# Optimization experiments

Hardware: AMD Instinct MI355X
Metric: run time of the kernel (lower is better)

Reference implementation:

```python
import jax, jax.numpy as jnp
import numpy as np

N = 262144          # total nodes in batched graph
B = 2048            # number of graphs
IN_DIM = 512        # in_dim == hidden_dim (required by GRUCell usage)
HID = 512
OUT_DIM = 128
TIMESTEPS = 2


def setup_inputs() -> dict:
    key = jax.random.key(0)
    ks = jax.random.split(key, 12)
    s = 0.02
    x = jax.random.normal(ks[0], (N, IN_DIM), dtype=jnp.float32)
    # sorted random segment ids: ragged graph sizes, node -> graph id
    segment_ids = jnp.sort(jax.random.randint(ks[1], (N,), 0, B, dtype=jnp.int32))
    return {
        "x": x,
        "segment_ids": segment_ids,
        "w_att_l": jax.random.normal(ks[2], (IN_DIM,), dtype=jnp.float32) * s,
        "w_att_r": jax.random.normal(ks[3], (IN_DIM,), dtype=jnp.float32) * s,
        "W_node": jax.random.normal(ks[4], (IN_DIM, HID), dtype=jnp.float32) * s,
        "W_ih": jax.random.normal(ks[5], (3 * HID, HID), dtype=jnp.float32) * s,
        "W_hh": jax.random.normal(ks[6], (3 * HID, HID), dtype=jnp.float32) * s,
        "b_ih": jax.random.normal(ks[7], (3 * HID,), dtype=jnp.float32) * s,
        "b_hh": jax.random.normal(ks[8], (3 * HID,), dtype=jnp.float32) * s,
        "W_lin": jax.random.normal(ks[9], (HID, OUT_DIM), dtype=jnp.float32) * s,
        "b_lin": jax.random.normal(ks[10], (OUT_DIM,), dtype=jnp.float32) * s,
    }


def _segment_softmax(alpha, seg, num_segments):
    # numerically stable per-graph softmax over nodes
    m = jax.ops.segment_max(alpha, seg, num_segments=num_segments)
    e = jnp.exp(alpha - m[seg])
    denom = jax.ops.segment_sum(e, seg, num_segments=num_segments)
    return e / denom[seg]


def _gru_cell(inp, h, W_ih, W_hh, b_ih, b_hh):
    gi = inp @ W_ih.T + b_ih          # [B, 3H]
    gh = h @ W_hh.T + b_hh            # [B, 3H]
    gi_r, gi_z, gi_n = jnp.split(gi, 3, axis=-1)
    gh_r, gh_z, gh_n = jnp.split(gh, 3, axis=-1)
    r = jax.nn.sigmoid(gi_r + gh_r)
    z = jax.nn.sigmoid(gi_z + gh_z)
    n = jnp.tanh(gi_n + r * gh_n)
    return (1.0 - z) * n + z * h


def reference(x, segment_ids, w_att_l, w_att_r, W_node, W_ih, W_hh, b_ih, b_hh, W_lin, b_lin):
    seg = segment_ids
    # SumPooling: per-graph sum of node features -> initial GRU hidden state
    out = jax.ops.segment_sum(x, seg, num_segments=B)      # [B, IN_DIM]
    # src_feats (x) are constant across timesteps -> precompute projections
    left_att = x @ w_att_l                                  # [N]
    h_neighbors = x @ W_node                                # [N, HID]
    for _ in range(TIMESTEPS):
        right_att = out @ w_att_r                           # [B]
        alpha = jax.nn.leaky_relu(left_att + right_att[seg], negative_slope=0.01)
        scores = _segment_softmax(alpha, seg, B)            # [N]
        msg = h_neighbors * scores[:, None]                 # [N, HID]
        gat_out = jax.ops.segment_sum(msg, seg, num_segments=B)  # [B, HID]
        h = jax.nn.elu(gat_out)
        # dropout is identity in eval mode
        out = jax.nn.silu(_gru_cell(h, out, W_ih, W_hh, b_ih, b_hh))
    return out @ W_lin + b_lin                              # [B, OUT_DIM]
```

## Files before the change

kernel.cpp:

```cpp
#include <hip/hip_runtime.h>
#include <hip/hip_bf16.h>
#include <cstdint>
#include <cstddef>

#define N_NODES 262144
#define NGRAPH  2048
#define DIM     512
#define HID3    1536
#define OUTD    128

typedef __attribute__((ext_vector_type(8))) short  short8;
typedef __attribute__((ext_vector_type(4))) float  floatx4;
typedef __attribute__((ext_vector_type(2))) float  floatx2;

__device__ inline unsigned short f2bf(float f) {
    union { float f; uint32_t u; } v; v.f = f;
    uint32_t u = v.u;
    return (unsigned short)((u + 0x7fffu + ((u >> 16) & 1u)) >> 16);
}
__device__ inline float bf2f(unsigned short h) {
    union { uint32_t u; float f; } v; v.u = ((uint32_t)h) << 16; return v.f;
}

__device__ __forceinline__ void gload_lds16(const void* g, void* l) {
    __builtin_amdgcn_global_load_lds((const __attribute__((address_space(1))) void*)g,
                                     (__attribute__((address_space(3))) void*)l, 16, 0, 0);
}

__device__ __forceinline__ int lbound(const int* __restrict__ seg, int b) {
    int lo = 0, hi = N_NODES;
    while (lo < hi) { int mid = (lo + hi) >> 1; if (seg[mid] < b) lo = mid + 1; else hi = mid; }
    return lo;
}

template<bool WRITE_XQ>
__global__ __launch_bounds__(256) void k_init(const float* __restrict__ x,
        const int* __restrict__ seg, const float* __restrict__ watl,
        const float* __restrict__ Wih, const float* __restrict__ Whh,
        const float* __restrict__ Wnode,
        float* __restrict__ left_att, float* __restrict__ hcur,
        unsigned short* __restrict__ hcur_bf, unsigned char* __restrict__ xq,
        unsigned short* __restrict__ Wihb, unsigned short* __restrict__ Whhb,
        unsigned short* __restrict__ WnT, int* __restrict__ starts) {
    int t = threadIdx.x;
    int bid = blockIdx.x;

    if (bid >= 3584) {
        __shared__ float tile[32][33];
        int idx = bid - 3584;
        int bx = idx >> 4, by = idx & 15;
        int tx = t & 31, ty = t >> 5;
        #pragma unroll
        for (int r = 0; r < 32; r += 8)
            tile[ty + r][tx] = Wnode[(size_t)(bx * 32 + ty + r) * DIM + by * 32 + tx];
        __syncthreads();
        #pragma unroll
        for (int r = 0; r < 32; r += 8)
            WnT[(size_t)(by * 32 + ty + r) * DIM + bx * 32 + tx] = f2bf(tile[tx][ty + r]);
        return;
    }
    if (bid >= 2048) {
        int isW2 = bid >= 2816;
        int i4 = (bid - (isW2 ? 2816 : 2048)) * 256 + t;
        const float* src = isW2 ? Whh : Wih;
        unsigned short* dst = isW2 ? Whhb : Wihb;
        floatx4 a = *reinterpret_cast<const floatx4*>(src + (size_t)i4 * 4);
        ushort4 o;
        o.x = f2bf(a[0]); o.y = f2bf(a[1]); o.z = f2bf(a[2]); o.w = f2bf(a[3]);
        *reinterpret_cast<ushort4*>(dst + (size_t)i4 * 4) = o;
        return;
    }

    __shared__ float wl[DIM];
    __shared__ float red[4 * DIM];
    int b = bid;
    wl[t] = watl[t]; wl[t + 256] = watl[t + 256];
    int s = lbound(seg, b), e = lbound(seg, b + 1);
    if (t == 0) {
        starts[b] = s;
        if (b == NGRAPH - 1) starts[NGRAPH] = e;
    }
    __syncthreads();
    int w = t >> 6, lane = t & 63;
    int f0 = lane * 4;
    float acc[8] = {0.f,0.f,0.f,0.f,0.f,0.f,0.f,0.f};

    auto proc = [&](int i, floatx4 v0, floatx4 v1) {
        acc[0] += v0[0]; acc[1] += v0[1]; acc[2] += v0[2]; acc[3] += v0[3];
        acc[4] += v1[0]; acc[5] += v1[1]; acc[6] += v1[2]; acc[7] += v1[3];
        float dot = v0[0]*wl[f0] + v0[1]*wl[f0+1] + v0[2]*wl[f0+2] + v0[3]*wl[f0+3]
                  + v1[0]*wl[256+f0] + v1[1]*wl[256+f0+1] + v1[2]*wl[256+f0+2] + v1[3]*wl[256+f0+3];
        #pragma unroll
        for (int off = 32; off > 0; off >>= 1) dot += __shfl_xor(dot, off);
        if (lane == 0) left_att[i] = dot;
        if constexpr (WRITE_XQ) {
            unsigned int q0 = (unsigned int)__builtin_amdgcn_cvt_pk_fp8_f32(v0[0], v0[1], 0, false);
            q0 = (unsigned int)__builtin_amdgcn_cvt_pk_fp8_f32(v0[2], v0[3], (int)q0, true);
            unsigned int q1 = (unsigned int)__builtin_amdgcn_cvt_pk_fp8_f32(v1[0], v1[1], 0, false);
            q1 = (unsigned int)__builtin_amdgcn_cvt_pk_fp8_f32(v1[2], v1[3], (int)q1, true);
            *reinterpret_cast<unsigned int*>(xq + (size_t)i * DIM + f0) = q0;
            *reinterpret_cast<unsigned int*>(xq + (size_t)i * DIM + 256 + f0) = q1;
        }
    };

    int i = s + w;
    for (; i + 4 < e; i += 8) {
        floatx4 a0 = __builtin_nontemporal_load(reinterpret_cast<const floatx4*>(x + (size_t)i * DIM + f0));
        floatx4 a1 = __builtin_nontemporal_load(reinterpret_cast<const floatx4*>(x + (size_t)i * DIM + 256 + f0));
        floatx4 b0 = __builtin_nontemporal_load(reinterpret_cast<const floatx4*>(x + (size_t)(i + 4) * DIM + f0));
        floatx4 b1 = __builtin_nontemporal_load(reinterpret_cast<const floatx4*>(x + (size_t)(i + 4) * DIM + 256 + f0));
        proc(i, a0, a1);
        proc(i + 4, b0, b1);
    }
    if (i < e) {
        floatx4 a0 = __builtin_nontemporal_load(reinterpret_cast<const floatx4*>(x + (size_t)i * DIM + f0));
        floatx4 a1 = __builtin_nontemporal_load(reinterpret_cast<const floatx4*>(x + (size_t)i * DIM + 256 + f0));
        proc(i, a0, a1);
    }

    #pragma unroll
    for (int j = 0; j < 4; j++) {
        red[w * DIM + f0 + j]       = acc[j];
        red[w * DIM + 256 + f0 + j] = acc[4 + j];
    }
    __syncthreads();
    float s0 = red[t]       + red[DIM + t]       + red[2*DIM + t]       + red[3*DIM + t];
    float s1 = red[256 + t] + red[DIM + 256 + t] + red[2*DIM + 256 + t] + red[3*DIM + 256 + t];
    hcur[(size_t)b * DIM + t] = s0;
    hcur[(size_t)b * DIM + 256 + t] = s1;
    hcur_bf[(size_t)b * DIM + t] = f2bf(s0);
    hcur_bf[(size_t)b * DIM + 256 + t] = f2bf(s1);
}

template<bool XQ, bool FUSE_GATE>
__global__ __launch_bounds__(256) void k_att(const float* __restrict__ x,
        const unsigned char* __restrict__ xq, const float* __restrict__ left,
        const int* __restrict__ starts, float* __restrict__ hcur,
        unsigned short* __restrict__ hcurbf,
        const float* __restrict__ gi, const float* __restrict__ gh,
        const float* __restrict__ bih, const float* __restrict__ bhh,
        const float* __restrict__ watr, unsigned short* __restrict__ swbf) {
    __shared__ float red[4 * DIM];
    __shared__ float rsh[4];
    __shared__ float rsm[4];
    __shared__ float rscal[4];
    int b = blockIdx.x, t = threadIdx.x;
    int w = t >> 6, lane = t & 63;

    float p;
    if constexpr (FUSE_GATE) {
        size_t gb = (size_t)b * HID3;
        float o01[2];
        #pragma unroll
        for (int half = 0; half < 2; ++half) {
            int j = t + half * 256;
            float gir = gi[gb + j]        + bih[j];
            float giz = gi[gb + 512 + j]  + bih[512 + j];
            float gin = gi[gb + 1024 + j] + bih[1024 + j];
            float ghr = gh[gb + j]        + bhh[j];
            float ghz = gh[gb + 512 + j]  + bhh[512 + j];
            float ghn = gh[gb + 1024 + j] + bhh[1024 + j];
            float rg = 1.0f / (1.0f + __expf(-(gir + ghr)));
            float zg = 1.0f / (1.0f + __expf(-(giz + ghz)));
            float nn = tanhf(gin + rg * ghn);
            float hp = hcur[(size_t)b * DIM + j];
            float nh = (1.0f - zg) * nn + zg * hp;
            float o = nh / (1.0f + __expf(-nh));
            hcur[(size_t)b * DIM + j] = o;
            hcurbf[(size_t)b * DIM + j] = f2bf(o);
            o01[half] = o;
        }
        p = o01[0] * watr[t] + o01[1] * watr[t + 256];
    } else {
        p = hcur[(size_t)b * DIM + t] * watr[t] + hcur[(size_t)b * DIM + 256 + t] * watr[256 + t];
    }
    #pragma unroll
    for (int off = 32; off > 0; off >>= 1) p += __shfl_xor(p, off);
    if (lane == 0) rsh[w] = p;
    int s = starts[b], e = starts[b + 1];
    __syncthreads();
    float ra = rsh[0] + rsh[1] + rsh[2] + rsh[3];

    float m = -1e30f;
    for (int i = s + t; i < e; i += 256) {
        float a = left[i] + ra; a = a >= 0.f ? a : 0.01f * a;
        m = fmaxf(m, a);
    }
    #pragma unroll
    for (int off = 32; off > 0; off >>= 1) m = fmaxf(m, __shfl_xor(m, off));
    if (lane == 0) rsm[w] = m;
    __syncthreads();
    m = fmaxf(fmaxf(rsm[0], rsm[1]), fmaxf(rsm[2], rsm[3]));

    float acc[8] = {0.f,0.f,0.f,0.f,0.f,0.f,0.f,0.f};
    float esum = 0.f;
    if constexpr (XQ) {
        int f0 = lane * 8;
        auto qacc = [&](uint2 q, float ev) {
            floatx2 p0 = __builtin_amdgcn_cvt_pk_f32_fp8((int)q.x, false);
            floatx2 p1 = __builtin_amdgcn_cvt_pk_f32_fp8((int)q.x, true);
            floatx2 p2 = __builtin_amdgcn_cvt_pk_f32_fp8((int)q.y, false);
            floatx2 p3 = __builtin_amdgcn_cvt_pk_f32_fp8((int)q.y, true);
            acc[0] += ev * p0[0]; acc[1] += ev * p0[1];
            acc[2] += ev * p1[0]; acc[3] += ev * p1[1];
            acc[4] += ev * p2[0]; acc[5] += ev * p2[1];
            acc[6] += ev * p3[0]; acc[7] += ev * p3[1];
        };
        int i = s + w;
        for (; i + 4 < e; i += 8) {
            uint2 q0 = *reinterpret_cast<const uint2*>(xq + (size_t)i * DIM + f0);
            uint2 q1 = *reinterpret_cast<const uint2*>(xq + (size_t)(i + 4) * DIM + f0);
            float a0 = left[i] + ra;     a0 = a0 >= 0.f ? a0 : 0.01f * a0;
            float a1 = left[i + 4] + ra; a1 = a1 >= 0.f ? a1 : 0.01f * a1;
            float e0 = __expf(a0 - m), e1 = __expf(a1 - m);
            esum += e0 + e1;
            qacc(q0, e0);
            qacc(q1, e1);
        }
        if (i < e) {
            uint2 q0 = *reinterpret_cast<const uint2*>(xq + (size_t)i * DIM + f0);
            float a0 = left[i] + ra; a0 = a0 >= 0.f ? a0 : 0.01f * a0;
            float e0 = __expf(a0 - m);
            esum += e0;
            qacc(q0, e0);
        }
        #pragma unroll
        for (int j = 0; j < 8; j++) red[w * DIM + f0 + j] = acc[j];
    } else {
        int f0 = lane * 4;
        for (int i = s + w; i < e; i += 4) {
            float a0 = left[i] + ra; a0 = a0 >= 0.f ? a0 : 0.01f * a0;
            float e0 = __expf(a0 - m);
            esum += e0;
            float4 v0 = *reinterpret_cast<const float4*>(x + (size_t)i * DIM + f0);
            float4 v1 = *reinterpret_cast<const float4*>(x + (size_t)i * DIM + 256 + f0);
            acc[0] += e0 * v0.x; acc[1] += e0 * v0.y; acc[2] += e0 * v0.z; acc[3] += e0 * v0.w;
            acc[4] += e0 * v1.x; acc[5] += e0 * v1.y; acc[6] += e0 * v1.z; acc[7] += e0 * v1.w;
        }
        #pragma unroll
        for (int j = 0; j < 4; j++) {
            red[w * DIM + f0 + j]       = acc[j];
            red[w * DIM + 256 + f0 + j] = acc[4 + j];
        }
    }
    #pragma unroll
    for (int off = 32; off > 0; off >>= 1) esum += __shfl_xor(esum, off);
    if (lane == 0) rscal[w] = esum;
    __syncthreads();
    float tot = rscal[0] + rscal[1] + rscal[2] + rscal[3];
    float inv = tot > 0.f ? 1.0f / tot : 0.0f;
    float s0 = (red[t]       + red[DIM + t]       + red[2*DIM + t]       + red[3*DIM + t])       * inv;
    float s1 = (red[256 + t] + red[DIM + 256 + t] + red[2*DIM + 256 + t] + red[3*DIM + 256 + t]) * inv;
    swbf[(size_t)b * DIM + t] = f2bf(s0);
    swbf[(size_t)b * DIM + 256 + t] = f2bf(s1);
}

__global__ __launch_bounds__(256, 2) void k_gemm(const unsigned short* __restrict__ A0,
        const unsigned short* __restrict__ Wt0, float* __restrict__ Cf0,
        unsigned short* __restrict__ Cb0, int Ncols0, int ny0,
        const unsigned short* __restrict__ A1, const unsigned short* __restrict__ Wt1,
        float* __restrict__ Cf1, unsigned short* __restrict__ Cb1, int Ncols1) {
    const int z = blockIdx.z;
    if (z == 0 && (int)blockIdx.y >= ny0) return;
    const unsigned short* A  = z ? A1  : A0;
    const unsigned short* Wt = z ? Wt1 : Wt0;
    float* Cf          = z ? Cf1 : Cf0;
    unsigned short* Cb = z ? Cb1 : Cb0;
    const int Ncols    = z ? Ncols1 : Ncols0;

    __shared__ __align__(16) unsigned short lA[2][128 * 64];
    __shared__ __align__(16) unsigned short lW[2][128 * 64];

    int t = threadIdx.x;
    int w = t >> 6, lane = t & 63;
    int wr = w >> 1, wc = w & 1;
    int mbase = blockIdx.x * 128;
    int nbase = blockIdx.y * 128;
    int fr = lane & 15, hi = lane >> 4;
    int swz_r = (fr & 7) << 4;

    int rbase = t >> 3;
    int cole = ((((t & 7) * 16) ^ ((rbase & 7) << 4)) >> 1);
    int ldsoff = t * 16;

    floatx4 acc[4][4];
    #pragma unroll
    for (int m = 0; m < 4; m++)
        #pragma unroll
        for (int n = 0; n < 4; n++) {
            acc[m][n][0] = 0.f; acc[m][n][1] = 0.f; acc[m][n][2] = 0.f; acc[m][n][3] = 0.f;
        }

    const unsigned short* gA = A  + (size_t)(mbase + rbase) * DIM + cole;
    const unsigned short* gW = Wt + (size_t)(nbase + rbase) * DIM + cole;

    auto stage = [&](int kk, int buf) {
        #pragma unroll
        for (int c = 0; c < 4; ++c) {
            gload_lds16(gA + (size_t)(c * 32) * DIM + kk, (char*)&lA[buf][0] + c * 4096 + ldsoff);
            gload_lds16(gW + (size_t)(c * 32) * DIM + kk, (char*)&lW[buf][0] + c * 4096 + ldsoff);
        }
    };

    stage(0, 0);
    __syncthreads();
    int cur = 0;
    for (int it = 0; it < 8; ++it) {
        if (it < 7) stage((it + 1) * 64, cur ^ 1);
        #pragma unroll
        for (int ks = 0; ks < 2; ++ks) {
            short8 af[4], bf[4];
            int bc = (ks * 64 + hi * 16) ^ swz_r;
            #pragma unroll
            for (int m = 0; m < 4; ++m) {
                int row = wr * 64 + m * 16 + fr;
                af[m] = *reinterpret_cast<const short8*>(&lA[cur][(row * 128 + bc) >> 1]);
            }
            #pragma unroll
            for (int n = 0; n < 4; ++n) {
                int row = wc * 64 + n * 16 + fr;
                bf[n] = *reinterpret_cast<const short8*>(&lW[cur][(row * 128 + bc) >> 1]);
            }
            #pragma unroll
            for (int m = 0; m < 4; ++m)
                #pragma unroll
                for (int n = 0; n < 4; ++n)
                    acc[m][n] = __builtin_amdgcn_mfma_f32_16x16x32_bf16(af[m], bf[n], acc[m][n], 0, 0, 0);
        }
        if (it < 7) __syncthreads();
        cur ^= 1;
    }

    int rq = hi * 4;
    #pragma unroll
    for (int m = 0; m < 4; m++) {
        #pragma unroll
        for (int n = 0; n < 4; n++) {
            int col = nbase + wc * 64 + n * 16 + fr;
            #pragma unroll
            for (int r = 0; r < 4; r++) {
                int row = mbase + wr * 64 + m * 16 + rq + r;
                float v = acc[m][n][r];
                if (Cb) {
                    v = v > 0.f ? v : (__expf(v) - 1.0f);
                    Cb[(size_t)row * Ncols + col] = f2bf(v);
                } else {
                    Cf[(size_t)row * Ncols + col] = v;
                }
            }
        }
    }
}

__global__ __launch_bounds__(128) void k_fin(const float* __restrict__ hcur,
        const float* __restrict__ gi, const float* __restrict__ gh,
        const float* __restrict__ bih, const float* __restrict__ bhh,
        const float* __restrict__ Wlin, const float* __restrict__ blin,
        float* __restrict__ out) {
    __shared__ float rows[16 * DIM];
    int t = threadIdx.x;
    int b0 = blockIdx.x * 16;
    for (int k = 0; k < 16; ++k) {
        int i4 = t + k * 128;
        int bl = i4 >> 7;
        int j  = (i4 & 127) << 2;
        size_t gb = (size_t)(b0 + bl) * HID3;
        floatx4 gir = *reinterpret_cast<const floatx4*>(gi + gb + j);
        floatx4 giz = *reinterpret_cast<const floatx4*>(gi + gb + 512 + j);
        floatx4 gin = *reinterpret_cast<const floatx4*>(gi + gb + 1024 + j);
        floatx4 ghr = *reinterpret_cast<const floatx4*>(gh + gb + j);
        floatx4 ghz = *reinterpret_cast<const floatx4*>(gh + gb + 512 + j);
        floatx4 ghn = *reinterpret_cast<const floatx4*>(gh + gb + 1024 + j);
        floatx4 bir = *reinterpret_cast<const floatx4*>(bih + j);
        floatx4 biz = *reinterpret_cast<const floatx4*>(bih + 512 + j);
        floatx4 bin = *reinterpret_cast<const floatx4*>(bih + 1024 + j);
        floatx4 bhr = *reinterpret_cast<const floatx4*>(bhh + j);
        floatx4 bhz = *reinterpret_cast<const floatx4*>(bhh + 512 + j);
        floatx4 bhn = *reinterpret_cast<const floatx4*>(bhh + 1024 + j);
        floatx4 hp  = *reinterpret_cast<const floatx4*>(hcur + (size_t)(b0 + bl) * DIM + j);
        floatx4 ov;
        #pragma unroll
        for (int r = 0; r < 4; r++) {
            float rg = 1.0f / (1.0f + __expf(-(gir[r] + bir[r] + ghr[r] + bhr[r])));
            float zg = 1.0f / (1.0f + __expf(-(giz[r] + biz[r] + ghz[r] + bhz[r])));
            float nn = tanhf(gin[r] + bin[r] + rg * (ghn[r] + bhn[r]));
            float nh = (1.0f - zg) * nn + zg * hp[r];
            ov[r] = nh / (1.0f + __expf(-nh));
        }
        *reinterpret_cast<floatx4*>(rows + (size_t)i4 * 4) = ov;
    }
    __syncthreads();
    float acc[16];
    #pragma unroll
    for (int r = 0; r < 16; r++) acc[r] = 0.f;
    #pragma unroll 4
    for (int k = 0; k < DIM; k++) {
        float wv = Wlin[k * OUTD + t];
        #pragma unroll
        for (int r = 0; r < 16; r++) acc[r] += rows[r * DIM + k] * wv;
    }
    float bl = blin[t];
    #pragma unroll
    for (int r = 0; r < 16; r++) out[(size_t)(b0 + r) * OUTD + t] = acc[r] + bl;
}

extern "C" void kernel_launch(void* const* d_in, const int* in_sizes, int n_in,
                              void* d_out, int out_size, void* d_ws, size_t ws_size,
                              hipStream_t stream) {
    const float* x     = (const float*)d_in[0];
    const int*   seg   = (const int*)d_in[1];
    const float* watl  = (const float*)d_in[2];
    const float* watr  = (const float*)d_in[3];
    const float* Wnode = (const float*)d_in[4];
    const float* Wih   = (const float*)d_in[5];
    const float* Whh   = (const float*)d_in[6];
    const float* bih   = (const float*)d_in[7];
    const float* bhh   = (const float*)d_in[8];
    const float* Wlin  = (const float*)d_in[9];
    const float* blin  = (const float*)d_in[10];
    float* out = (float*)d_out;

    char* ws = (char*)d_ws;
    size_t off = 0;
    auto alloc = [&](size_t bytes) -> void* {
        void* p = ws + off;
        off += bytes;
        off = (off + 255) & ~(size_t)255;
        return p;
    };
    float*          left    = (float*)          alloc((size_t)N_NODES * sizeof(float));
    float*          hcur    = (float*)          alloc((size_t)NGRAPH * DIM * sizeof(float));
    unsigned short* hcurbf  = (unsigned short*) alloc((size_t)NGRAPH * DIM * 2);
    unsigned short* hgbf    = (unsigned short*) alloc((size_t)NGRAPH * DIM * 2);
    unsigned short* swbf    = (unsigned short*) alloc((size_t)NGRAPH * DIM * 2);
    float*          gi      = (float*)          alloc((size_t)NGRAPH * HID3 * sizeof(float));
    float*          gh      = (float*)          alloc((size_t)NGRAPH * HID3 * sizeof(float));
    unsigned short* WnT     = (unsigned short*) alloc((size_t)DIM * DIM * 2);
    unsigned short* Wihb    = (unsigned short*) alloc((size_t)HID3 * DIM * 2);
    unsigned short* Whhb    = (unsigned short*) alloc((size_t)HID3 * DIM * 2);
    int*            starts  = (int*)            alloc((NGRAPH + 1) * sizeof(int));
    unsigned char*  xq      = (unsigned char*)(ws + off);
    bool use_xq = (off + (size_t)N_NODES * DIM) <= ws_size;

    if (use_xq)
        k_init<true ><<<3840, 256, 0, stream>>>(x, seg, watl, Wih, Whh, Wnode,
                left, hcur, hcurbf, xq, Wihb, Whhb, WnT, starts);
    else
        k_init<false><<<3840, 256, 0, stream>>>(x, seg, watl, Wih, Whh, Wnode,
                left, hcur, hcurbf, nullptr, Wihb, Whhb, WnT, starts);

    for (int ts = 0; ts < 2; ts++) {
        if (use_xq) {
            if (ts == 0)
                k_att<true , false><<<NGRAPH, 256, 0, stream>>>(x, xq, left, starts,
                        hcur, hcurbf, gi, gh, bih, bhh, watr, swbf);
            else
                k_att<true , true ><<<NGRAPH, 256, 0, stream>>>(x, xq, left, starts,
                        hcur, hcurbf, gi, gh, bih, bhh, watr, swbf);
        } else {
            if (ts == 0)
                k_att<false, false><<<NGRAPH, 256, 0, stream>>>(x, xq, left, starts,
                        hcur, hcurbf, gi, gh, bih, bhh, watr, swbf);
            else
                k_att<false, true ><<<NGRAPH, 256, 0, stream>>>(x, xq, left, starts,
                        hcur, hcurbf, gi, gh, bih, bhh, watr, swbf);
        }
        k_gemm<<<dim3(NGRAPH / 128, HID3 / 128, 2), 256, 0, stream>>>(
            swbf, WnT, nullptr, hgbf, DIM, DIM / 128,
            hcurbf, Whhb, gh, nullptr, HID3);
        k_gemm<<<dim3(NGRAPH / 128, HID3 / 128, 1), 256, 0, stream>>>(
            hgbf, Wihb, gi, nullptr, HID3, HID3 / 128,
            nullptr, nullptr, nullptr, nullptr, 0);
    }
    k_fin<<<NGRAPH / 16, 128, 0, stream>>>(hcur, gi, gh, bih, bhh, Wlin, blin, out);
}
```

Baseline: 300.9 us.

## Fuse first attention pass into init kernel and store GRU gates as bf16

The first timestep's attention (softmax plus weighted aggregation) moves into the init kernel's per-graph branch. It reuses left-attention scores cached in LDS and the freshly computed pooled sum, which removes one full k_att launch and its re-read of left scores. The GEMM outputs for the gi and gh gate pre-activations are now written as bf16 instead of fp32, which halves that traffic in the GEMMs, k_att and k_fin. The cost is extra LDS and register pressure in k_init and lower precision on the gate pre-activations.

```diff
diff --git a/kernel.cpp b/kernel.cpp
--- a/kernel.cpp
+++ b/kernel.cpp
@@ -8,6 +8,7 @@
 #define DIM     512
 #define HID3    1536
 #define OUTD    128
+#define MAXROWS 384
 
 typedef __attribute__((ext_vector_type(8))) short  short8;
 typedef __attribute__((ext_vector_type(4))) float  floatx4;
@@ -36,12 +37,14 @@
 template<bool WRITE_XQ>
 __global__ __launch_bounds__(256) void k_init(const float* __restrict__ x,
         const int* __restrict__ seg, const float* __restrict__ watl,
+        const float* __restrict__ watr,
         const float* __restrict__ Wih, const float* __restrict__ Whh,
         const float* __restrict__ Wnode,
         float* __restrict__ left_att, float* __restrict__ hcur,
         unsigned short* __restrict__ hcur_bf, unsigned char* __restrict__ xq,
         unsigned short* __restrict__ Wihb, unsigned short* __restrict__ Whhb,
-        unsigned short* __restrict__ WnT, int* __restrict__ starts) {
+        unsigned short* __restrict__ WnT, int* __restrict__ starts,
+        unsigned short* __restrict__ swbf) {
     int t = threadIdx.x;
     int bid = blockIdx.x;
 
@@ -73,6 +76,8 @@
 
     __shared__ float wl[DIM];
     __shared__ float red[4 * DIM];
+    __shared__ float lleft[MAXROWS];
+    __shared__ float rsh[4], rsm[4], rscal[4];
     int b = bid;
     wl[t] = watl[t]; wl[t + 256] = watl[t + 256];
     int s = lbound(seg, b), e = lbound(seg, b + 1);
@@ -92,7 +97,10 @@
                   + v1[0]*wl[256+f0] + v1[1]*wl[256+f0+1] + v1[2]*wl[256+f0+2] + v1[3]*wl[256+f0+3];
         #pragma unroll
         for (int off = 32; off > 0; off >>= 1) dot += __shfl_xor(dot, off);
-        if (lane == 0) left_att[i] = dot;
+        if (lane == 0) {
+            left_att[i] = dot;
+            if (i - s < MAXROWS) lleft[i - s] = dot;
+        }
         if constexpr (WRITE_XQ) {
             unsigned int q0 = (unsigned int)__builtin_amdgcn_cvt_pk_fp8_f32(v0[0], v0[1], 0, false);
             q0 = (unsigned int)__builtin_amdgcn_cvt_pk_fp8_f32(v0[2], v0[3], (int)q0, true);
@@ -130,50 +138,114 @@
     hcur[(size_t)b * DIM + 256 + t] = s1;
     hcur_bf[(size_t)b * DIM + t] = f2bf(s0);
     hcur_bf[(size_t)b * DIM + 256 + t] = f2bf(s1);
-}
-
-template<bool XQ, bool FUSE_GATE>
+
+    float p = s0 * watr[t] + s1 * watr[t + 256];
+    #pragma unroll
+    for (int off = 32; off > 0; off >>= 1) p += __shfl_xor(p, off);
+    if (lane == 0) rsh[w] = p;
+    __threadfence_block();
+    __syncthreads();
+    float ra = rsh[0] + rsh[1] + rsh[2] + rsh[3];
+    int els = e - s;
+    bool uselds = els <= MAXROWS;
+
+    float m = -1e30f;
+    for (int r = t; r < els; r += 256) {
+        float lv = uselds ? lleft[r] : left_att[s + r];
+        float a = lv + ra; a = a >= 0.f ? a : 0.01f * a;
+        m = fmaxf(m, a);
+    }
+    #pragma unroll
+    for (int off = 32; off > 0; off >>= 1) m = fmaxf(m, __shfl_xor(m, off));
+    if (lane == 0) rsm[w] = m;
+    __syncthreads();
+    m = fmaxf(fmaxf(rsm[0], rsm[1]), fmaxf(rsm[2], rsm[3]));
+
+    float wacc[8] = {0.f,0.f,0.f,0.f,0.f,0.f,0.f,0.f};
+    float esum = 0.f;
+    if constexpr (WRITE_XQ) {
+        int g0 = lane * 8;
+        for (int r = s + w; r < e; r += 4) {
+            uint2 q = *reinterpret_cast<const uint2*>(xq + (size_t)r * DIM + g0);
+            float lv = uselds ? lleft[r - s] : left_att[r];
+            float a = lv + ra; a = a >= 0.f ? a : 0.01f * a;
+            float e0 = __expf(a - m);
+            esum += e0;
+            floatx2 p0 = __builtin_amdgcn_cvt_pk_f32_fp8((int)q.x, false);
+            floatx2 p1 = __builtin_amdgcn_cvt_pk_f32_fp8((int)q.x, true);
+            floatx2 p2 = __builtin_amdgcn_cvt_pk_f32_fp8((int)q.y, false);
+            floatx2 p3 = __builtin_amdgcn_cvt_pk_f32_fp8((int)q.y, true);
+            wacc[0] += e0 * p0[0]; wacc[1] += e0 * p0[1];
+            wacc[2] += e0 * p1[0]; wacc[3] += e0 * p1[1];
+            wacc[4] += e0 * p2[0]; wacc[5] += e0 * p2[1];
+            wacc[6] += e0 * p3[0]; wacc[7] += e0 * p3[1];
+        }
+        #pragma unroll
+        for (int j = 0; j < 8; j++) red[w * DIM + g0 + j] = wacc[j];
+    } else {
+        for (int r = s + w; r < e; r += 4) {
+            float lv = uselds ? lleft[r - s] : left_att[r];
+            float a = lv + ra; a = a >= 0.f ? a : 0.01f * a;
+            float e0 = __expf(a - m);
+            esum += e0;
+            floatx4 v0 = *reinterpret_cast<const floatx4*>(x + (size_t)r * DIM + f0);
+            floatx4 v1 = *reinterpret_cast<const floatx4*>(x + (size_t)r * DIM + 256 + f0);
+            wacc[0] += e0 * v0[0]; wacc[1] += e0 * v0[1]; wacc[2] += e0 * v0[2]; wacc[3] += e0 * v0[3];
+            wacc[4] += e0 * v1[0]; wacc[5] += e0 * v1[1]; wacc[6] += e0 * v1[2]; wacc[7] += e0 * v1[3];
+        }
+        #pragma unroll
+        for (int j = 0; j < 4; j++) {
+            red[w * DIM + f0 + j]       = wacc[j];
+            red[w * DIM + 256 + f0 + j] = wacc[4 + j];
+        }
+    }
+    #pragma unroll
+    for (int off = 32; off > 0; off >>= 1) esum += __shfl_xor(esum, off);
+    if (lane == 0) rscal[w] = esum;
+    __syncthreads();
+    float tot = rscal[0] + rscal[1] + rscal[2] + rscal[3];
+    float inv = tot > 0.f ? 1.0f / tot : 0.0f;
+    float o0 = (red[t]       + red[DIM + t]       + red[2*DIM + t]       + red[3*DIM + t])       * inv;
+    float o1 = (red[256 + t] + red[DIM + 256 + t] + red[2*DIM + 256 + t] + red[3*DIM + 256 + t]) * inv;
+    swbf[(size_t)b * DIM + t] = f2bf(o0);
+    swbf[(size_t)b * DIM + 256 + t] = f2bf(o1);
+}
+
+template<bool XQ>
 __global__ __launch_bounds__(256) void k_att(const float* __restrict__ x,
         const unsigned char* __restrict__ xq, const float* __restrict__ left,
         const int* __restrict__ starts, float* __restrict__ hcur,
         unsigned short* __restrict__ hcurbf,
-        const float* __restrict__ gi, const float* __restrict__ gh,
+        const unsigned short* __restrict__ gib, const unsigned short* __restrict__ ghb,
         const float* __restrict__ bih, const float* __restrict__ bhh,
         const float* __restrict__ watr, unsigned short* __restrict__ swbf) {
     __shared__ float red[4 * DIM];
-    __shared__ float rsh[4];
-    __shared__ float rsm[4];
-    __shared__ float rscal[4];
+    __shared__ float rsh[4], rsm[4], rscal[4];
     int b = blockIdx.x, t = threadIdx.x;
     int w = t >> 6, lane = t & 63;
 
-    float p;
-    if constexpr (FUSE_GATE) {
-        size_t gb = (size_t)b * HID3;
-        float o01[2];
-        #pragma unroll
-        for (int half = 0; half < 2; ++half) {
-            int j = t + half * 256;
-            float gir = gi[gb + j]        + bih[j];
-            float giz = gi[gb + 512 + j]  + bih[512 + j];
-            float gin = gi[gb + 1024 + j] + bih[1024 + j];
-            float ghr = gh[gb + j]        + bhh[j];
-            float ghz = gh[gb + 512 + j]  + bhh[512 + j];
-            float ghn = gh[gb + 1024 + j] + bhh[1024 + j];
-            float rg = 1.0f / (1.0f + __expf(-(gir + ghr)));
-            float zg = 1.0f / (1.0f + __expf(-(giz + ghz)));
-            float nn = tanhf(gin + rg * ghn);
-            float hp = hcur[(size_t)b * DIM + j];
-            float nh = (1.0f - zg) * nn + zg * hp;
-            float o = nh / (1.0f + __expf(-nh));
-            hcur[(size_t)b * DIM + j] = o;
-            hcurbf[(size_t)b * DIM + j] = f2bf(o);
-            o01[half] = o;
-        }
-        p = o01[0] * watr[t] + o01[1] * watr[t + 256];
-    } else {
-        p = hcur[(size_t)b * DIM + t] * watr[t] + hcur[(size_t)b * DIM + 256 + t] * watr[256 + t];
-    }
+    size_t gb = (size_t)b * HID3;
+    float o01[2];
+    #pragma unroll
+    for (int half = 0; half < 2; ++half) {
+        int j = t + half * 256;
+        float gir = bf2f(gib[gb + j])        + bih[j];
+        float giz = bf2f(gib[gb + 512 + j])  + bih[512 + j];
+        float gin = bf2f(gib[gb + 1024 + j]) + bih[1024 + j];
+        float ghr = bf2f(ghb[gb + j])        + bhh[j];
+        float ghz = bf2f(ghb[gb + 512 + j])  + bhh[512 + j];
+        float ghn = bf2f(ghb[gb + 1024 + j]) + bhh[1024 + j];
+        float rg = 1.0f / (1.0f + __expf(-(gir + ghr)));
+        float zg = 1.0f / (1.0f + __expf(-(giz + ghz)));
+        float nn = tanhf(gin + rg * ghn);
+        float hp = hcur[(size_t)b * DIM + j];
+        float nh = (1.0f - zg) * nn + zg * hp;
+        float o = nh / (1.0f + __expf(-nh));
+        hcur[(size_t)b * DIM + j] = o;
+        hcurbf[(size_t)b * DIM + j] = f2bf(o);
+        o01[half] = o;
+    }
+    float p = o01[0] * watr[t] + o01[1] * watr[t + 256];
     #pragma unroll
     for (int off = 32; off > 0; off >>= 1) p += __shfl_xor(p, off);
     if (lane == 0) rsh[w] = p;
@@ -256,17 +328,17 @@
 }
 
 __global__ __launch_bounds__(256, 2) void k_gemm(const unsigned short* __restrict__ A0,
-        const unsigned short* __restrict__ Wt0, float* __restrict__ Cf0,
-        unsigned short* __restrict__ Cb0, int Ncols0, int ny0,
+        const unsigned short* __restrict__ Wt0, void* __restrict__ C0,
+        int mode0, int Ncols0, int ny0,
         const unsigned short* __restrict__ A1, const unsigned short* __restrict__ Wt1,
-        float* __restrict__ Cf1, unsigned short* __restrict__ Cb1, int Ncols1) {
+        void* __restrict__ C1, int mode1, int Ncols1) {
     const int z = blockIdx.z;
     if (z == 0 && (int)blockIdx.y >= ny0) return;
     const unsigned short* A  = z ? A1  : A0;
     const unsigned short* Wt = z ? Wt1 : Wt0;
-    float* Cf          = z ? Cf1 : Cf0;
-    unsigned short* Cb = z ? Cb1 : Cb0;
-    const int Ncols    = z ? Ncols1 : Ncols0;
+    void* C         = z ? C1 : C0;
+    const int mode  = z ? mode1 : mode0;
+    const int Ncols = z ? Ncols1 : Ncols0;
 
     __shared__ __align__(16) unsigned short lA[2][128 * 64];
     __shared__ __align__(16) unsigned short lW[2][128 * 64];
@@ -341,11 +413,11 @@
             for (int r = 0; r < 4; r++) {
                 int row = mbase + wr * 64 + m * 16 + rq + r;
                 float v = acc[m][n][r];
-                if (Cb) {
-                    v = v > 0.f ? v : (__expf(v) - 1.0f);
-                    Cb[(size_t)row * Ncols + col] = f2bf(v);
+                if (mode == 0) {
+                    ((float*)C)[(size_t)row * Ncols + col] = v;
                 } else {
-                    Cf[(size_t)row * Ncols + col] = v;
+                    if (mode == 1) v = v > 0.f ? v : (__expf(v) - 1.0f);
+                    ((unsigned short*)C)[(size_t)row * Ncols + col] = f2bf(v);
                 }
             }
         }
@@ -353,7 +425,7 @@
 }
 
 __global__ __launch_bounds__(128) void k_fin(const float* __restrict__ hcur,
-        const float* __restrict__ gi, const float* __restrict__ gh,
+        const unsigned short* __restrict__ gib, const unsigned short* __restrict__ ghb,
         const float* __restrict__ bih, const float* __restrict__ bhh,
         const float* __restrict__ Wlin, const float* __restrict__ blin,
         float* __restrict__ out) {
@@ -365,12 +437,12 @@
         int bl = i4 >> 7;
         int j  = (i4 & 127) << 2;
         size_t gb = (size_t)(b0 + bl) * HID3;
-        floatx4 gir = *reinterpret_cast<const floatx4*>(gi + gb + j);
-        floatx4 giz = *reinterpret_cast<const floatx4*>(gi + gb + 512 + j);
-        floatx4 gin = *reinterpret_cast<const floatx4*>(gi + gb + 1024 + j);
-        floatx4 ghr = *reinterpret_cast<const floatx4*>(gh + gb + j);
-        floatx4 ghz = *reinterpret_cast<const floatx4*>(gh + gb + 512 + j);
-        floatx4 ghn = *reinterpret_cast<const floatx4*>(gh + gb + 1024 + j);
+        ushort4 gir4 = *reinterpret_cast<const ushort4*>(gib + gb + j);
+        ushort4 giz4 = *reinterpret_cast<const ushort4*>(gib + gb + 512 + j);
+        ushort4 gin4 = *reinterpret_cast<const ushort4*>(gib + gb + 1024 + j);
+        ushort4 ghr4 = *reinterpret_cast<const ushort4*>(ghb + gb + j);
+        ushort4 ghz4 = *reinterpret_cast<const ushort4*>(ghb + gb + 512 + j);
+        ushort4 ghn4 = *reinterpret_cast<const ushort4*>(ghb + gb + 1024 + j);
         floatx4 bir = *reinterpret_cast<const floatx4*>(bih + j);
         floatx4 biz = *reinterpret_cast<const floatx4*>(bih + 512 + j);
         floatx4 bin = *reinterpret_cast<const floatx4*>(bih + 1024 + j);
@@ -379,11 +451,17 @@
         floatx4 bhn = *reinterpret_cast<const floatx4*>(bhh + 1024 + j);
         floatx4 hp  = *reinterpret_cast<const floatx4*>(hcur + (size_t)(b0 + bl) * DIM + j);
         floatx4 ov;
+        const unsigned short* girp = &gir4.x;
+        const unsigned short* gizp = &giz4.x;
+        const unsigned short* ginp = &gin4.x;
+        const unsigned short* ghrp = &ghr4.x;
+        const unsigned short* ghzp = &ghz4.x;
+        const unsigned short* ghnp = &ghn4.x;
         #pragma unroll
         for (int r = 0; r < 4; r++) {
-            float rg = 1.0f / (1.0f + __expf(-(gir[r] + bir[r] + ghr[r] + bhr[r])));
-            float zg = 1.0f / (1.0f + __expf(-(giz[r] + biz[r] + ghz[r] + bhz[r])));
-            float nn = tanhf(gin[r] + bin[r] + rg * (ghn[r] + bhn[r]));
+            float rg = 1.0f / (1.0f + __expf(-(bf2f(girp[r]) + bir[r] + bf2f(ghrp[r]) + bhr[r])));
+            float zg = 1.0f / (1.0f + __expf(-(bf2f(gizp[r]) + biz[r] + bf2f(ghzp[r]) + bhz[r])));
+            float nn = tanhf(bf2f(ginp[r]) + bin[r] + rg * (bf2f(ghnp[r]) + bhn[r]));
             float nh = (1.0f - zg) * nn + zg * hp[r];
             ov[r] = nh / (1.0f + __expf(-nh));
         }
@@ -433,8 +511,8 @@
     unsigned short* hcurbf  = (unsigned short*) alloc((size_t)NGRAPH * DIM * 2);
     unsigned short* hgbf    = (unsigned short*) alloc((size_t)NGRAPH * DIM * 2);
     unsigned short* swbf    = (unsigned short*) alloc((size_t)NGRAPH * DIM * 2);
-    float*          gi      = (float*)          alloc((size_t)NGRAPH * HID3 * sizeof(float));
-    float*          gh      = (float*)          alloc((size_t)NGRAPH * HID3 * sizeof(float));
+    unsigned short* gib     = (unsigned short*) alloc((size_t)NGRAPH * HID3 * 2);
+    unsigned short* ghb     = (unsigned short*) alloc((size_t)NGRAPH * HID3 * 2);
     unsigned short* WnT     = (unsigned short*) alloc((size_t)DIM * DIM * 2);
     unsigned short* Wihb    = (unsigned short*) alloc((size_t)HID3 * DIM * 2);
     unsigned short* Whhb    = (unsigned short*) alloc((size_t)HID3 * DIM * 2);
@@ -443,34 +521,27 @@
     bool use_xq = (off + (size_t)N_NODES * DIM) <= ws_size;
 
     if (use_xq)
-        k_init<true ><<<3840, 256, 0, stream>>>(x, seg, watl, Wih, Whh, Wnode,
-                left, hcur, hcurbf, xq, Wihb, Whhb, WnT, starts);
+        k_init<true ><<<3840, 256, 0, stream>>>(x, seg, watl, watr, Wih, Whh, Wnode,
+                left, hcur, hcurbf, xq, Wihb, Whhb, WnT, starts, swbf);
     else
-        k_init<false><<<3840, 256, 0, stream>>>(x, seg, watl, Wih, Whh, Wnode,
-                left, hcur, hcurbf, nullptr, Wihb, Whhb, WnT, starts);
+        k_init<false><<<3840, 256, 0, stream>>>(x, seg, watl, watr, Wih, Whh, Wnode,
+                left, hcur, hcurbf, nullptr, Wihb, Whhb, WnT, starts, swbf);
 
     for (int ts = 0; ts < 2; ts++) {
-        if (use_xq) {
-            if (ts == 0)
-                k_att<true , false><<<NGRAPH, 256, 0, stream>>>(x, xq, left, starts,
-                        hcur, hcurbf, gi, gh, bih, bhh, watr, swbf);
+        if (ts == 1) {
+            if (use_xq)
+                k_att<true ><<<NGRAPH, 256, 0, stream>>>(x, xq, left, starts,
+                        hcur, hcurbf, gib, ghb, bih, bhh, watr, swbf);
             else
-                k_att<true , true ><<<NGRAPH, 256, 0, stream>>>(x, xq, left, starts,
-                        hcur, hcurbf, gi, gh, bih, bhh, watr, swbf);
-        } else {
-            if (ts == 0)
-                k_att<false, false><<<NGRAPH, 256, 0, stream>>>(x, xq, left, starts,
-                        hcur, hcurbf, gi, gh, bih, bhh, watr, swbf);
-            else
-                k_att<false, true ><<<NGRAPH, 256, 0, stream>>>(x, xq, left, starts,
-                        hcur, hcurbf, gi, gh, bih, bhh, watr, swbf);
+                k_att<false><<<NGRAPH, 256, 0, stream>>>(x, xq, left, starts,
+                        hcur, hcurbf, gib, ghb, bih, bhh, watr, swbf);
         }
         k_gemm<<<dim3(NGRAPH / 128, HID3 / 128, 2), 256, 0, stream>>>(
-            swbf, WnT, nullptr, hgbf, DIM, DIM / 128,
-            hcurbf, Whhb, gh, nullptr, HID3);
+            swbf, WnT, hgbf, 1, DIM, DIM / 128,
+            hcurbf, Whhb, ghb, 2, HID3);
         k_gemm<<<dim3(NGRAPH / 128, HID3 / 128, 1), 256, 0, stream>>>(
-            hgbf, Wihb, gi, nullptr, HID3, HID3 / 128,
-            nullptr, nullptr, nullptr, nullptr, 0);
-    }
-    k_fin<<<NGRAPH / 16, 128, 0, stream>>>(hcur, gi, gh, bih, bhh, Wlin, blin, out);
-}
+            hgbf, Wihb, gib, 2, HID3, HID3 / 128,
+            nullptr, nullptr, nullptr, 0, 0);
+    }
+    k_fin<<<NGRAPH / 16, 128, 0, stream>>>(hcur, gib, ghb, bih, bhh, Wlin, blin, out);
+}
```

Measured after the change: 318.5 us. 5.9% more time.

## Store GRU gate GEMM outputs in bf16 and regroup GEMM launches

Applied to the files above, without the earlier changes.

The gi/gh gate pre-activations are now written as bf16 instead of fp32, and the GRU update in k_att and k_fin reads bf16 and converts. The GEMM launches are regrouped: the W_node GEMM with ELU runs alone, then the W_ih and W_hh GEMMs share one launch along z, so each launch has uniform work. This halves gate-tensor memory traffic, but the gate values lose precision.

```diff
diff --git a/kernel.cpp b/kernel.cpp
--- a/kernel.cpp
+++ b/kernel.cpp
@@ -137,13 +137,11 @@
         const unsigned char* __restrict__ xq, const float* __restrict__ left,
         const int* __restrict__ starts, float* __restrict__ hcur,
         unsigned short* __restrict__ hcurbf,
-        const float* __restrict__ gi, const float* __restrict__ gh,
+        const unsigned short* __restrict__ gib, const unsigned short* __restrict__ ghb,
         const float* __restrict__ bih, const float* __restrict__ bhh,
         const float* __restrict__ watr, unsigned short* __restrict__ swbf) {
     __shared__ float red[4 * DIM];
-    __shared__ float rsh[4];
-    __shared__ float rsm[4];
-    __shared__ float rscal[4];
+    __shared__ float rsh[4], rsm[4], rscal[4];
     int b = blockIdx.x, t = threadIdx.x;
     int w = t >> 6, lane = t & 63;
 
@@ -154,12 +152,12 @@
         #pragma unroll
         for (int half = 0; half < 2; ++half) {
             int j = t + half * 256;
-            float gir = gi[gb + j]        + bih[j];
-            float giz = gi[gb + 512 + j]  + bih[512 + j];
-            float gin = gi[gb + 1024 + j] + bih[1024 + j];
-            float ghr = gh[gb + j]        + bhh[j];
-            float ghz = gh[gb + 512 + j]  + bhh[512 + j];
-            float ghn = gh[gb + 1024 + j] + bhh[1024 + j];
+            float gir = bf2f(gib[gb + j])        + bih[j];
+            float giz = bf2f(gib[gb + 512 + j])  + bih[512 + j];
+            float gin = bf2f(gib[gb + 1024 + j]) + bih[1024 + j];
+            float ghr = bf2f(ghb[gb + j])        + bhh[j];
+            float ghz = bf2f(ghb[gb + 512 + j])  + bhh[512 + j];
+            float ghn = bf2f(ghb[gb + 1024 + j]) + bhh[1024 + j];
             float rg = 1.0f / (1.0f + __expf(-(gir + ghr)));
             float zg = 1.0f / (1.0f + __expf(-(giz + ghz)));
             float nn = tanhf(gin + rg * ghn);
@@ -256,17 +254,16 @@
 }
 
 __global__ __launch_bounds__(256, 2) void k_gemm(const unsigned short* __restrict__ A0,
-        const unsigned short* __restrict__ Wt0, float* __restrict__ Cf0,
-        unsigned short* __restrict__ Cb0, int Ncols0, int ny0,
+        const unsigned short* __restrict__ Wt0, unsigned short* __restrict__ C0,
+        int mode0, int Ncols0,
         const unsigned short* __restrict__ A1, const unsigned short* __restrict__ Wt1,
-        float* __restrict__ Cf1, unsigned short* __restrict__ Cb1, int Ncols1) {
+        unsigned short* __restrict__ C1, int mode1, int Ncols1) {
     const int z = blockIdx.z;
-    if (z == 0 && (int)blockIdx.y >= ny0) return;
     const unsigned short* A  = z ? A1  : A0;
     const unsigned short* Wt = z ? Wt1 : Wt0;
-    float* Cf          = z ? Cf1 : Cf0;
-    unsigned short* Cb = z ? Cb1 : Cb0;
-    const int Ncols    = z ? Ncols1 : Ncols0;
+    unsigned short* C = z ? C1 : C0;
+    const int mode  = z ? mode1 : mode0;
+    const int Ncols = z ? Ncols1 : Ncols0;
 
     __shared__ __align__(16) unsigned short lA[2][128 * 64];
     __shared__ __align__(16) unsigned short lW[2][128 * 64];
@@ -341,19 +338,15 @@
             for (int r = 0; r < 4; r++) {
                 int row = mbase + wr * 64 + m * 16 + rq + r;
                 float v = acc[m][n][r];
-                if (Cb) {
-                    v = v > 0.f ? v : (__expf(v) - 1.0f);
-                    Cb[(size_t)row * Ncols + col] = f2bf(v);
-                } else {
-                    Cf[(size_t)row * Ncols + col] = v;
-                }
+                if (mode == 1) v = v > 0.f ? v : (__expf(v) - 1.0f);
+                C[(size_t)row * Ncols + col] = f2bf(v);
             }
         }
     }
 }
 
 __global__ __launch_bounds__(128) void k_fin(const float* __restrict__ hcur,
-        const float* __restrict__ gi, const float* __restrict__ gh,
+        const unsigned short* __restrict__ gib, const unsigned short* __restrict__ ghb,
         const float* __restrict__ bih, const float* __restrict__ bhh,
         const float* __restrict__ Wlin, const float* __restrict__ blin,
         float* __restrict__ out) {
@@ -365,12 +358,12 @@
         int bl = i4 >> 7;
         int j  = (i4 & 127) << 2;
         size_t gb = (size_t)(b0 + bl) * HID3;
-        floatx4 gir = *reinterpret_cast<const floatx4*>(gi + gb + j);
-        floatx4 giz = *reinterpret_cast<const floatx4*>(gi + gb + 512 + j);
-        floatx4 gin = *reinterpret_cast<const floatx4*>(gi + gb + 1024 + j);
-        floatx4 ghr = *reinterpret_cast<const floatx4*>(gh + gb + j);
-        floatx4 ghz = *reinterpret_cast<const floatx4*>(gh + gb + 512 + j);
-        floatx4 ghn = *reinterpret_cast<const floatx4*>(gh + gb + 1024 + j);
+        ushort4 gir4 = *reinterpret_cast<const ushort4*>(gib + gb + j);
+        ushort4 giz4 = *reinterpret_cast<const ushort4*>(gib + gb + 512 + j);
+        ushort4 gin4 = *reinterpret_cast<const ushort4*>(gib + gb + 1024 + j);
+        ushort4 ghr4 = *reinterpret_cast<const ushort4*>(ghb + gb + j);
+        ushort4 ghz4 = *reinterpret_cast<const ushort4*>(ghb + gb + 512 + j);
+        ushort4 ghn4 = *reinterpret_cast<const ushort4*>(ghb + gb + 1024 + j);
         floatx4 bir = *reinterpret_cast<const floatx4*>(bih + j);
         floatx4 biz = *reinterpret_cast<const floatx4*>(bih + 512 + j);
         floatx4 bin = *reinterpret_cast<const floatx4*>(bih + 1024 + j);
@@ -379,11 +372,17 @@
         floatx4 bhn = *reinterpret_cast<const floatx4*>(bhh + 1024 + j);
         floatx4 hp  = *reinterpret_cast<const floatx4*>(hcur + (size_t)(b0 + bl) * DIM + j);
         floatx4 ov;
+        const unsigned short* girp = &gir4.x;
+        const unsigned short* gizp = &giz4.x;
+        const unsigned short* ginp = &gin4.x;
+        const unsigned short* ghrp = &ghr4.x;
+        const unsigned short* ghzp = &ghz4.x;
+        const unsigned short* ghnp = &ghn4.x;
         #pragma unroll
         for (int r = 0; r < 4; r++) {
-            float rg = 1.0f / (1.0f + __expf(-(gir[r] + bir[r] + ghr[r] + bhr[r])));
-            float zg = 1.0f / (1.0f + __expf(-(giz[r] + biz[r] + ghz[r] + bhz[r])));
-            float nn = tanhf(gin[r] + bin[r] + rg * (ghn[r] + bhn[r]));
+            float rg = 1.0f / (1.0f + __expf(-(bf2f(girp[r]) + bir[r] + bf2f(ghrp[r]) + bhr[r])));
+            float zg = 1.0f / (1.0f + __expf(-(bf2f(gizp[r]) + biz[r] + bf2f(ghzp[r]) + bhz[r])));
+            float nn = tanhf(bf2f(ginp[r]) + bin[r] + rg * (bf2f(ghnp[r]) + bhn[r]));
             float nh = (1.0f - zg) * nn + zg * hp[r];
             ov[r] = nh / (1.0f + __expf(-nh));
         }
@@ -433,8 +432,8 @@
     unsigned short* hcurbf  = (unsigned short*) alloc((size_t)NGRAPH * DIM * 2);
     unsigned short* hgbf    = (unsigned short*) alloc((size_t)NGRAPH * DIM * 2);
     unsigned short* swbf    = (unsigned short*) alloc((size_t)NGRAPH * DIM * 2);
-    float*          gi      = (float*)          alloc((size_t)NGRAPH * HID3 * sizeof(float));
-    float*          gh      = (float*)          alloc((size_t)NGRAPH * HID3 * sizeof(float));
+    unsigned short* gib     = (unsigned short*) alloc((size_t)NGRAPH * HID3 * 2);
+    unsigned short* ghb     = (unsigned short*) alloc((size_t)NGRAPH * HID3 * 2);
     unsigned short* WnT     = (unsigned short*) alloc((size_t)DIM * DIM * 2);
     unsigned short* Wihb    = (unsigned short*) alloc((size_t)HID3 * DIM * 2);
     unsigned short* Whhb    = (unsigned short*) alloc((size_t)HID3 * DIM * 2);
@@ -453,24 +452,24 @@
         if (use_xq) {
             if (ts == 0)
                 k_att<true , false><<<NGRAPH, 256, 0, stream>>>(x, xq, left, starts,
-                        hcur, hcurbf, gi, gh, bih, bhh, watr, swbf);
+                        hcur, hcurbf, gib, ghb, bih, bhh, watr, swbf);
             else
                 k_att<true , true ><<<NGRAPH, 256, 0, stream>>>(x, xq, left, starts,
-                        hcur, hcurbf, gi, gh, bih, bhh, watr, swbf);
+                        hcur, hcurbf, gib, ghb, bih, bhh, watr, swbf);
         } else {
             if (ts == 0)
                 k_att<false, false><<<NGRAPH, 256, 0, stream>>>(x, xq, left, starts,
-                        hcur, hcurbf, gi, gh, bih, bhh, watr, swbf);
+                        hcur, hcurbf, gib, ghb, bih, bhh, watr, swbf);
             else
                 k_att<false, true ><<<NGRAPH, 256, 0, stream>>>(x, xq, left, starts,
-                        hcur, hcurbf, gi, gh, bih, bhh, watr, swbf);
-        }
+                        hcur, hcurbf, gib, ghb, bih, bhh, watr, swbf);
+        }
+        k_gemm<<<dim3(NGRAPH / 128, DIM / 128, 1), 256, 0, stream>>>(
+            swbf, WnT, hgbf, 1, DIM,
+            nullptr, nullptr, nullptr, 0, 0);
         k_gemm<<<dim3(NGRAPH / 128, HID3 / 128, 2), 256, 0, stream>>>(
-            swbf, WnT, nullptr, hgbf, DIM, DIM / 128,
-            hcurbf, Whhb, gh, nullptr, HID3);
-        k_gemm<<<dim3(NGRAPH / 128, HID3 / 128, 1), 256, 0, stream>>>(
-            hgbf, Wihb, gi, nullptr, HID3, HID3 / 128,
-            nullptr, nullptr, nullptr, nullptr, 0);
-    }
-    k_fin<<<NGRAPH / 16, 128, 0, stream>>>(hcur, gi, gh, bih, bhh, Wlin, blin, out);
-}
+            hgbf, Wihb, gib, 2, HID3,
+            hcurbf, Whhb, ghb, 2, HID3);
+    }
+    k_fin<<<NGRAPH / 16, 128, 0, stream>>>(hcur, gib, ghb, bih, bhh, Wlin, blin, out);
+}
```

Measured after the change: 292.9 us. 1.03x faster.
